# Kernel optimization log

Measured on AMD Instinct MI355X. Metric: run time of the kernel, lower is better.

## Reference

```python
import jax, jax.numpy as jnp
import numpy as np

B, S, D = 1, 2048, 2048
H, KV, HD = 16, 8, 128
GROUP = H // KV
INTER = 6144
L = 2
VOCAB = 32000
EPS = 1e-6
THETA = 10000.0


def _rope_tables(seq_len, head_dim, theta):
    inv_freq = 1.0 / theta ** (np.arange(0, head_dim, 2, dtype=np.float32) / head_dim)
    pos = np.arange(seq_len, dtype=np.float32)
    ang = pos[:, None] * inv_freq[None, :]
    ang = np.concatenate([ang, ang], axis=1)  # [S, HD]
    return jnp.asarray(np.cos(ang)), jnp.asarray(np.sin(ang))


def setup_inputs() -> dict:
    key = jax.random.key(0)
    ks = jax.random.split(key, 16)
    sd = 0.02
    inp = {}
    inp['input_ids'] = jax.random.randint(ks[0], (B, S), 0, VOCAB, dtype=jnp.int32)
    inp['mask'] = jnp.triu(jnp.ones((S, S), dtype=bool), k=1)  # True = masked (future)
    cos, sin = _rope_tables(S, HD, THETA)
    inp['cos'], inp['sin'] = cos, sin
    inp['embed'] = jax.random.normal(ks[1], (VOCAB, D), jnp.float32) * sd
    # torch Linear convention: weight [out, in], y = x @ W.T
    inp['q_w'] = jax.random.normal(ks[2], (L, H * HD, D), jnp.float32) * sd
    inp['k_w'] = jax.random.normal(ks[3], (L, KV * HD, D), jnp.float32) * sd
    inp['v_w'] = jax.random.normal(ks[4], (L, KV * HD, D), jnp.float32) * sd
    inp['o_w'] = jax.random.normal(ks[5], (L, D, H * HD), jnp.float32) * sd
    inp['qn_scale'] = jnp.ones((L, HD), jnp.float32)
    inp['kn_scale'] = jnp.ones((L, HD), jnp.float32)
    inp['ln1_scale'] = jnp.ones((L, D), jnp.float32)
    inp['ln2_scale'] = jnp.ones((L, D), jnp.float32)
    inp['gate_w'] = jax.random.normal(ks[6], (L, INTER, D), jnp.float32) * sd
    inp['up_w'] = jax.random.normal(ks[7], (L, INTER, D), jnp.float32) * sd
    inp['down_w'] = jax.random.normal(ks[8], (L, D, INTER), jnp.float32) * sd
    return inp


def rms_norm(x, scale, eps=EPS):
    xf = x.astype(jnp.float32)
    var = jnp.mean(xf * xf, axis=-1, keepdims=True)
    return (xf * jax.lax.rsqrt(var + eps) * scale).astype(x.dtype)


def apply_rope(x, cos, sin):
    # x: [B, heads, S, HD]
    s = x.shape[2]
    hd = x.shape[-1]
    x1, x2 = x[..., : hd // 2], x[..., hd // 2:]
    rotated = jnp.concatenate([-x2, x1], axis=-1)
    return x * cos[None, None, :s] + rotated * sin[None, None, :s]


def decoder_layer(h, p, mask, cos, sin):
    (q_w, k_w, v_w, o_w, qn, kn, ln1, ln2, gate_w, up_w, down_w) = p
    b, s, _ = h.shape
    x = rms_norm(h, ln1)
    q = (x @ q_w.T).reshape(b, s, H, HD).transpose(0, 2, 1, 3)   # [B,H,S,HD]
    k = (x @ k_w.T).reshape(b, s, KV, HD).transpose(0, 2, 1, 3)  # [B,KV,S,HD]
    v = (x @ v_w.T).reshape(b, s, KV, HD).transpose(0, 2, 1, 3)
    q = rms_norm(q, qn)
    k = rms_norm(k, kn)
    q = apply_rope(q, cos, sin)
    k = apply_rope(k, cos, sin)
    kr = jnp.repeat(k, GROUP, axis=1)  # GQA head expansion
    vr = jnp.repeat(v, GROUP, axis=1)
    scores = jnp.einsum('bhqd,bhkd->bhqk', q, kr) / jnp.sqrt(jnp.float32(HD))
    scores = jnp.where(mask[None, None], -jnp.inf, scores)
    attn = jax.nn.softmax(scores, axis=-1)
    ctx = jnp.einsum('bhqk,bhkd->bhqd', attn, vr)
    ctx = ctx.transpose(0, 2, 1, 3).reshape(b, s, H * HD)
    h = h + ctx @ o_w.T
    x = rms_norm(h, ln2)
    mlp = (jax.nn.silu(x @ gate_w.T) * (x @ up_w.T)) @ down_w.T
    return h + mlp


def reference(input_ids, mask, cos, sin, embed, q_w, k_w, v_w, o_w,
              qn_scale, kn_scale, ln1_scale, ln2_scale, gate_w, up_w, down_w):
    h = embed[input_ids]  # [B, S, D]
    params = (q_w, k_w, v_w, o_w, qn_scale, kn_scale, ln1_scale, ln2_scale,
              gate_w, up_w, down_w)

    def body(carry, p):
        return decoder_layer(carry, p, mask, cos, sin), None

    h, _ = jax.lax.scan(body, h, params)
    return h
```

## Files before the change

### kernel.cpp

```cpp
#include <hip/hip_runtime.h>
#include <hip/hip_bf16.h>

static constexpr int SEQ   = 2048;
static constexpr int DM    = 2048;
static constexpr int NHEAD = 16;
static constexpr int NKVH  = 8;
static constexpr int HDIM  = 128;
static constexpr int FFN   = 6144;
static constexpr int NLAYER = 2;
static constexpr float EPSV = 1e-6f;
static constexpr int QKVN  = NHEAD * HDIM + 2 * NKVH * HDIM;

typedef __attribute__((ext_vector_type(8))) short bf16x8;
typedef __attribute__((ext_vector_type(4))) float f32x4;

__device__ __forceinline__ float wave_sum(float v) {
#pragma unroll
    for (int o = 32; o > 0; o >>= 1) v += __shfl_xor(v, o);
    return v;
}

__device__ __forceinline__ void gload16(const void* g, void* l) {
    __builtin_amdgcn_global_load_lds(
        (const __attribute__((address_space(1))) void*)g,
        (__attribute__((address_space(3))) void*)l,
        16, 0, 0);
}

__global__ void embed_k(const int* __restrict__ ids, const float* __restrict__ emb,
                        float* __restrict__ h) {
    const int s = blockIdx.x;
    const long src = (long)ids[s] * DM;
    for (int t = threadIdx.x; t < DM; t += 256)
        h[(long)s * DM + t] = emb[src + t];
}

__global__ void rmsnorm_k(const float* __restrict__ in, const float* __restrict__ g,
                          __hip_bfloat16* __restrict__ out) {
    const int row = blockIdx.x;
    const float* r = in + (long)row * DM;
    const int tid = threadIdx.x;
    float v[8];
    float ss = 0.f;
#pragma unroll
    for (int t = 0; t < 8; ++t) { v[t] = r[tid + t * 256]; ss += v[t] * v[t]; }
    ss = wave_sum(ss);
    __shared__ float sp[4];
    if ((tid & 63) == 0) sp[tid >> 6] = ss;
    __syncthreads();
    ss = sp[0] + sp[1] + sp[2] + sp[3];
    const float inv = rsqrtf(ss * (1.f / DM) + EPSV);
    __hip_bfloat16* o_ = out + (long)row * DM;
#pragma unroll
    for (int t = 0; t < 8; ++t) {
        const int j = tid + t * 256;
        o_[j] = __float2bfloat16(v[t] * inv * g[j]);
    }
}

__global__ void rmsnorm_res4_k(const __hip_bfloat16* __restrict__ part, long n,
                               float* __restrict__ h, const float* __restrict__ g,
                               __hip_bfloat16* __restrict__ x) {
    const int row = blockIdx.x;
    const int tid = threadIdx.x;
    const long base = (long)row * DM + tid * 8;
    float v[8];
    *(float4*)&v[0] = *(const float4*)(h + base);
    *(float4*)&v[4] = *(const float4*)(h + base + 4);
#pragma unroll
    for (int z = 0; z < 4; ++z) {
        union { bf16x8 vv; __hip_bfloat16 e[8]; } p;
        p.vv = *(const bf16x8*)(part + (long)z * n + base);
#pragma unroll
        for (int j = 0; j < 8; ++j) v[j] += __bfloat162float(p.e[j]);
    }
    *(float4*)(h + base) = *(float4*)&v[0];
    *(float4*)(h + base + 4) = *(float4*)&v[4];
    float ss = 0.f;
#pragma unroll
    for (int j = 0; j < 8; ++j) ss += v[j] * v[j];
    ss = wave_sum(ss);
    __shared__ float sp[4];
    if ((tid & 63) == 0) sp[tid >> 6] = ss;
    __syncthreads();
    ss = sp[0] + sp[1] + sp[2] + sp[3];
    const float inv = rsqrtf(ss * (1.f / DM) + EPSV);
    const float4 g0 = *(const float4*)(g + tid * 8);
    const float4 g1 = *(const float4*)(g + tid * 8 + 4);
    union { bf16x8 vv; __hip_bfloat16 e[8]; } o;
    o.e[0] = __float2bfloat16(v[0] * inv * g0.x); o.e[1] = __float2bfloat16(v[1] * inv * g0.y);
    o.e[2] = __float2bfloat16(v[2] * inv * g0.z); o.e[3] = __float2bfloat16(v[3] * inv * g0.w);
    o.e[4] = __float2bfloat16(v[4] * inv * g1.x); o.e[5] = __float2bfloat16(v[5] * inv * g1.y);
    o.e[6] = __float2bfloat16(v[6] * inv * g1.z); o.e[7] = __float2bfloat16(v[7] * inv * g1.w);
    *(bf16x8*)(x + base) = o.vv;
}

__global__ void red4res_k(const __hip_bfloat16* __restrict__ p, long n, float* __restrict__ h) {
    const long i = ((long)blockIdx.x * 256 + threadIdx.x) * 8;
    float v[8];
    *(float4*)&v[0] = *(const float4*)(h + i);
    *(float4*)&v[4] = *(const float4*)(h + i + 4);
#pragma unroll
    for (int z = 0; z < 4; ++z) {
        union { bf16x8 vv; __hip_bfloat16 e[8]; } b;
        b.vv = *(const bf16x8*)(p + (long)z * n + i);
#pragma unroll
        for (int j = 0; j < 8; ++j) v[j] += __bfloat162float(b.e[j]);
    }
    *(float4*)(h + i) = *(float4*)&v[0];
    *(float4*)(h + i + 4) = *(float4*)&v[4];
}

__global__ void qknorm_rope_k(const __hip_bfloat16* __restrict__ in, long zStride, int inOff,
                              const float* __restrict__ ns,
                              const float* __restrict__ cosT, const float* __restrict__ sinT,
                              __hip_bfloat16* __restrict__ out, int nheads) {
    const int idx = blockIdx.x * 4 + (threadIdx.x >> 6);
    const int lane = threadIdx.x & 63;
    const int s = idx / nheads;
    const int hh = idx - s * nheads;
    const long base = (long)s * QKVN + inOff + hh * HDIM;
    const float x1 = __bfloat162float(in[base + lane]) + __bfloat162float(in[zStride + base + lane]);
    const float x2 = __bfloat162float(in[base + lane + 64]) + __bfloat162float(in[zStride + base + lane + 64]);
    float ss = wave_sum(x1 * x1 + x2 * x2);
    const float inv = rsqrtf(ss * (1.f / HDIM) + EPSV);
    const float n1 = x1 * inv * ns[lane];
    const float n2 = x2 * inv * ns[lane + 64];
    const float c1 = cosT[s * HDIM + lane],      c2 = cosT[s * HDIM + 64 + lane];
    const float s1 = sinT[s * HDIM + lane],      s2 = sinT[s * HDIM + 64 + lane];
    __hip_bfloat16* w = out + ((long)hh * SEQ + s) * HDIM;
    w[lane]      = __float2bfloat16(n1 * c1 - n2 * s1);
    w[lane + 64] = __float2bfloat16(n2 * c2 + n1 * s2);
}

__global__ void vtrans_k(const __hip_bfloat16* __restrict__ vf, long zStride, int colOff,
                         __hip_bfloat16* __restrict__ vt) {
    __shared__ float tile[64][65];
    const int s0 = blockIdx.x * 64, d0 = blockIdx.y * 64, kv = blockIdx.z;
    const int lane = threadIdx.x & 63, part = threadIdx.x >> 6;
    for (int r = part; r < 64; r += 4) {
        const long idx = (long)(s0 + r) * QKVN + colOff + kv * HDIM + d0 + lane;
        tile[r][lane] = __bfloat162float(vf[idx]) + __bfloat162float(vf[zStride + idx]);
    }
    __syncthreads();
    for (int r = part; r < 64; r += 4)
        vt[((long)kv * HDIM + d0 + r) * SEQ + s0 + lane] = __float2bfloat16(tile[lane][r]);
}

__global__ void silu_red2_k(const __hip_bfloat16* __restrict__ p, long n,
                            __hip_bfloat16* __restrict__ out) {
    const long i = ((long)blockIdx.x * 256 + threadIdx.x) * 8;
    union { bf16x8 v; __hip_bfloat16 e[8]; } g0, g1, u0, u1, o;
    g0.v = *(const bf16x8*)(p + i);
    g1.v = *(const bf16x8*)(p + n + i);
    u0.v = *(const bf16x8*)(p + 2 * n + i);
    u1.v = *(const bf16x8*)(p + 3 * n + i);
#pragma unroll
    for (int j = 0; j < 8; ++j) {
        const float g = __bfloat162float(g0.e[j]) + __bfloat162float(g1.e[j]);
        const float u = __bfloat162float(u0.e[j]) + __bfloat162float(u1.e[j]);
        const float sv = g / (1.f + __expf(-g));
        o.e[j] = __float2bfloat16(sv * u);
    }
    *(bf16x8*)(out + i) = o.v;
}

__global__ __launch_bounds__(256)
void flash_k(const __hip_bfloat16* __restrict__ qb, const __hip_bfloat16* __restrict__ kb,
             const __hip_bfloat16* __restrict__ vt, __hip_bfloat16* __restrict__ ctx) {
    __shared__ __align__(16) char ks[2][16384];
    __shared__ __align__(16) char vs[2][16384];
    __shared__ __align__(16) char ps[4][2048];

    const int tid = threadIdx.x;
    const int lane = tid & 63;
    const int wid = tid >> 6;
    const int l15 = lane & 15;
    const int l4 = lane >> 4;

    const int h = blockIdx.y;
    const int kvh = h >> 1;
    const float scale = 0.0883883476483184405f;

    auto stageK = [&](int buf, int kt) {
        const __hip_bfloat16* kg = kb + ((long)kvh * SEQ + kt * 64) * HDIM;
#pragma unroll
        for (int i = 0; i < 4; ++i) {
            const int c = i * 256 + tid;
            const int r = c >> 4, s = c & 15;
            gload16(kg + (long)r * HDIM + ((s ^ (r & 7)) * 8), ks[buf] + c * 16);
        }
    };
    auto stageV = [&](int buf, int kt) {
        const __hip_bfloat16* vg = vt + (long)kvh * HDIM * SEQ + kt * 64;
#pragma unroll
        for (int i = 0; i < 4; ++i) {
            const int c = i * 256 + tid;
            const int r = c >> 3, s = c & 7;
            gload16(vg + (long)r * SEQ + ((s ^ (r & 7)) * 8), vs[buf] + c * 16);
        }
    };

#pragma unroll
    for (int half = 0; half < 2; ++half) {
        const int x = half ? 31 - blockIdx.x : blockIdx.x;
        const int q0 = x * 64;
        const int nkt = x + 1;

        bf16x8 aq[4];
        {
            const __hip_bfloat16* qg = qb + ((long)h * SEQ + q0 + wid * 16 + l15) * HDIM + l4 * 8;
#pragma unroll
            for (int kk = 0; kk < 4; ++kk) aq[kk] = *(const bf16x8*)(qg + kk * 32);
        }

        float mreg[4], lreg[4];
#pragma unroll
        for (int j = 0; j < 4; ++j) { mreg[j] = -3.0e38f; lreg[j] = 0.f; }
        f32x4 oacc[8];
#pragma unroll
        for (int n = 0; n < 8; ++n) oacc[n] = (f32x4){0.f, 0.f, 0.f, 0.f};

        stageK(0, 0); stageV(0, 0);
        asm volatile("s_waitcnt vmcnt(0)" ::: "memory");
        __builtin_amdgcn_s_barrier();

        for (int kt = 0; kt < nkt; ++kt) {
            const int cur = kt & 1;
            if (kt + 1 < nkt) { stageK(cur ^ 1, kt + 1); stageV(cur ^ 1, kt + 1); }

            f32x4 sac[4];
#pragma unroll
            for (int n = 0; n < 4; ++n) sac[n] = (f32x4){0.f, 0.f, 0.f, 0.f};
            __builtin_amdgcn_s_setprio(1);
#pragma unroll
            for (int kk = 0; kk < 4; ++kk) {
#pragma unroll
                for (int n = 0; n < 4; ++n) {
                    const int r = n * 16 + l15;
                    const bf16x8 bk = *(const bf16x8*)(ks[cur] + r * 256 + (((kk * 4 + l4) ^ (r & 7)) << 4));
                    sac[n] = __builtin_amdgcn_mfma_f32_16x16x32_bf16(aq[kk], bk, sac[n], 0, 0, 0);
                }
            }
            __builtin_amdgcn_s_setprio(0);

            const bool diag = (kt + 1 == nkt);
            float mnj[4], alj[4];
#pragma unroll
            for (int j = 0; j < 4; ++j) {
                float mx = -3.0e38f;
#pragma unroll
                for (int n = 0; n < 4; ++n) {
                    float v = sac[n][j] * scale;
                    if (diag && (n * 16 + l15 > wid * 16 + l4 * 4 + j)) v = -3.0e38f;
                    sac[n][j] = v;
                    mx = fmaxf(mx, v);
                }
#pragma unroll
                for (int o = 1; o < 16; o <<= 1) mx = fmaxf(mx, __shfl_xor(mx, o));
                const float mn = fmaxf(mreg[j], mx);
                mnj[j] = mn;
                alj[j] = __expf(mreg[j] - mn);
                mreg[j] = mn;
            }
#pragma unroll
            for (int j = 0; j < 4; ++j) {
                float rs = 0.f;
#pragma unroll
                for (int n = 0; n < 4; ++n) {
                    const float e = __expf(sac[n][j] - mnj[j]);
                    sac[n][j] = e;
                    rs += e;
                }
#pragma unroll
                for (int o = 1; o < 16; o <<= 1) rs += __shfl_xor(rs, o);
                lreg[j] = lreg[j] * alj[j] + rs;
#pragma unroll
                for (int n2 = 0; n2 < 8; ++n2) oacc[n2][j] *= alj[j];
            }

            char* pw = ps[wid];
#pragma unroll
            for (int n = 0; n < 4; ++n)
#pragma unroll
                for (int j = 0; j < 4; ++j) {
                    const int r = l4 * 4 + j;
                    const int col = n * 16 + l15;
                    *(__hip_bfloat16*)(pw + r * 128 + (((col >> 3) ^ (r & 7)) << 4) + (col & 7) * 2) =
                        __float2bfloat16(sac[n][j]);
                }
            asm volatile("s_waitcnt lgkmcnt(0)" ::: "memory");
            __builtin_amdgcn_sched_barrier(0);
            __builtin_amdgcn_s_setprio(1);
#pragma unroll
            for (int kk = 0; kk < 2; ++kk) {
                const bf16x8 ap = *(const bf16x8*)(pw + l15 * 128 + (((kk * 4 + l4) ^ (l15 & 7)) << 4));
#pragma unroll
                for (int n2 = 0; n2 < 8; ++n2) {
                    const int r = n2 * 16 + l15;
                    const bf16x8 bv = *(const bf16x8*)(vs[cur] + r * 128 + (((kk * 4 + l4) ^ (r & 7)) << 4));
                    oacc[n2] = __builtin_amdgcn_mfma_f32_16x16x32_bf16(ap, bv, oacc[n2], 0, 0, 0);
                }
            }
            __builtin_amdgcn_s_setprio(0);

            asm volatile("s_waitcnt vmcnt(0)" ::: "memory");
            __builtin_amdgcn_s_barrier();
        }

#pragma unroll
        for (int j = 0; j < 4; ++j) {
            const float inv = 1.f / lreg[j];
            const long rowb = (long)(q0 + wid * 16 + l4 * 4 + j) * (NHEAD * HDIM) + h * HDIM;
#pragma unroll
            for (int n2 = 0; n2 < 8; ++n2)
                ctx[rowb + n2 * 16 + l15] = __float2bfloat16(oacc[n2][j] * inv);
        }
    }
}

template <int ZSEL>
__global__ __launch_bounds__(512, 2)
void g8p(const __hip_bfloat16* __restrict__ A,
         const float* __restrict__ Ba, const float* __restrict__ Bb, const float* __restrict__ Bc,
         __hip_bfloat16* __restrict__ C, int kLen, int ldA, int ldB, int ldC,
         int seg1, int seg2, long cZStride, int kZStride, int zDiv) {
    __shared__ __align__(16) char sA[2][2][16384];
    __shared__ __align__(16) char sB[2][2][16384];

    const int tid = threadIdx.x;
    const int lane = tid & 63;
    const int wid = tid >> 6;
    const int wr = wid >> 2;
    const int wc = wid & 3;
    const int l15 = lane & 15;
    const int l4 = lane >> 4;

    const int row0 = blockIdx.y * 256;
    const int col0 = blockIdx.x * 256;
    const int z = blockIdx.z;

    const float* B;
    int colB;
    if (ZSEL) {
        B = (z / zDiv) ? Bb : Ba; colB = col0;
    } else {
        if (col0 >= seg2)      { B = Bc; colB = col0 - seg2; }
        else if (col0 >= seg1) { B = Bb; colB = col0 - seg1; }
        else                   { B = Ba; colB = col0; }
    }
    const long cOff = (long)z * cZStride;
    const int k0z = (z % zDiv) * kZStride;
    const int nk = kLen / 64;

    f32x4 acc[8][4];
#pragma unroll
    for (int m = 0; m < 8; ++m)
#pragma unroll
        for (int n = 0; n < 4; ++n)
            acc[m][n] = (f32x4){0.f, 0.f, 0.f, 0.f};

    auto stageA = [&](int half, int kt) {
        const __hip_bfloat16* base = A + (long)(row0 + half * 128) * ldA;
        char* dst = sA[kt & 1][half];
        const int k0 = k0z + kt * 64;
#pragma unroll
        for (int i = 0; i < 2; ++i) {
            const int c = i * 512 + tid;
            const int r = c >> 3, s = c & 7;
            gload16(base + (long)r * ldA + k0 + ((s ^ (r & 7)) * 8), dst + c * 16);
        }
    };
    auto loadB = [&](float4* rb, int half, int kt) {
        const int k0 = k0z + kt * 64;
        const float* base = B + (long)(colB + half * 128) * ldB + k0;
#pragma unroll
        for (int i = 0; i < 2; ++i) {
            const int sidx = i * 512 + tid;
            const int r = sidx >> 3, q = sidx & 7;
            const float* p = base + (long)r * ldB + q * 8;
            rb[i * 2]     = *(const float4*)p;
            rb[i * 2 + 1] = *(const float4*)(p + 4);
        }
    };
    auto writeB = [&](const float4* rb, int half, int kt) {
        char* dst = sB[kt & 1][half];
#pragma unroll
        for (int i = 0; i < 2; ++i) {
            const int sidx = i * 512 + tid;
            const int r = sidx >> 3, q = sidx & 7;
            union { bf16x8 v; __hip_bfloat16 e[8]; } u;
            const float* f = (const float*)&rb[i * 2];
#pragma unroll
            for (int j = 0; j < 8; ++j) u.e[j] = __float2bfloat16(f[j]);
            *(bf16x8*)(dst + (r * 8 + (q ^ (r & 7))) * 16) = u.v;
        }
    };

    auto readA = [&](int buf, int p, int mm, int ks) -> bf16x8 {
        const int r = p * 32 + mm * 16 + l15;
        const int q = ks * 4 + l4;
        return *(const bf16x8*)(sA[buf][wr] + r * 128 + ((q ^ (r & 7)) << 4));
    };
    auto readB = [&](int buf, int nn, int ks) -> bf16x8 {
        const int r = (wc & 1) * 64 + nn * 16 + l15;
        const int q = ks * 4 + l4;
        return *(const bf16x8*)(sB[buf][wc >> 1] + r * 128 + ((q ^ (r & 7)) << 4));
    };

    float4 rb0[4], rb1[4];
    loadB(rb0, 0, 0);
    stageA(0, 0); stageA(1, 0);
    asm volatile("s_waitcnt vmcnt(4)" ::: "memory");
    writeB(rb0, 0, 0);
    loadB(rb1, 1, 0);
    asm volatile("s_waitcnt vmcnt(0)" ::: "memory");
    writeB(rb1, 1, 0);
    if (nk > 1) { loadB(rb0, 0, 1); loadB(rb1, 1, 1); }
    asm volatile("s_waitcnt lgkmcnt(0)" ::: "memory");
    __builtin_amdgcn_sched_barrier(0);
    __builtin_amdgcn_s_barrier();

    bf16x8 bfrag[4][2];
    for (int t = 0; t < nk; ++t) {
        const int cur = t & 1;

        {
            bf16x8 a0[2][2], a1[2][2];
            a0[0][0] = readA(cur, 0, 0, 0); a0[0][1] = readA(cur, 0, 0, 1);
            a0[1][0] = readA(cur, 0, 1, 0); a0[1][1] = readA(cur, 0, 1, 1);
            a1[0][0] = readA(cur, 1, 0, 0); a1[0][1] = readA(cur, 1, 0, 1);
            a1[1][0] = readA(cur, 1, 1, 0); a1[1][1] = readA(cur, 1, 1, 1);
#pragma unroll
            for (int n = 0; n < 4; ++n) {
                bfrag[n][0] = readB(cur, n, 0);
                bfrag[n][1] = readB(cur, n, 1);
            }
            if (t + 1 < nk) {
                writeB(rb0, 0, t + 1);
                writeB(rb1, 1, t + 1);
                stageA(0, t + 1);
                stageA(1, t + 1);
            }
            asm volatile("s_waitcnt lgkmcnt(8)" ::: "memory");
            __builtin_amdgcn_sched_barrier(0);
            __builtin_amdgcn_s_barrier();
            asm volatile("s_waitcnt lgkmcnt(0)" ::: "memory");
            __builtin_amdgcn_sched_barrier(0);

            __builtin_amdgcn_s_setprio(1);
#pragma unroll
            for (int ks = 0; ks < 2; ++ks) {
#pragma unroll
                for (int mm = 0; mm < 2; ++mm)
#pragma unroll
                    for (int n = 0; n < 4; ++n)
                        acc[mm][n] = __builtin_amdgcn_mfma_f32_16x16x32_bf16(
                            a0[mm][ks], bfrag[n][ks], acc[mm][n], 0, 0, 0);
#pragma unroll
                for (int mm = 0; mm < 2; ++mm)
#pragma unroll
                    for (int n = 0; n < 4; ++n)
                        acc[2 + mm][n] = __builtin_amdgcn_mfma_f32_16x16x32_bf16(
                            a1[mm][ks], bfrag[n][ks], acc[2 + mm][n], 0, 0, 0);
            }
            __builtin_amdgcn_s_setprio(0);
            __builtin_amdgcn_sched_barrier(0);
            __builtin_amdgcn_s_barrier();
        }

        {
            bf16x8 a2[2][2], a3[2][2];
            a2[0][0] = readA(cur, 2, 0, 0); a2[0][1] = readA(cur, 2, 0, 1);
            a2[1][0] = readA(cur, 2, 1, 0); a2[1][1] = readA(cur, 2, 1, 1);
            a3[0][0] = readA(cur, 3, 0, 0); a3[0][1] = readA(cur, 3, 0, 1);
            a3[1][0] = readA(cur, 3, 1, 0); a3[1][1] = readA(cur, 3, 1, 1);
            if (t + 2 < nk) {
                loadB(rb0, 0, t + 2);
                loadB(rb1, 1, t + 2);
            }
            __builtin_amdgcn_sched_barrier(0);
            if (t + 2 < nk)      asm volatile("s_waitcnt vmcnt(8)" ::: "memory");
            else if (t + 1 < nk) asm volatile("s_waitcnt vmcnt(0)" ::: "memory");
            __builtin_amdgcn_s_barrier();
            asm volatile("s_waitcnt lgkmcnt(0)" ::: "memory");
            __builtin_amdgcn_sched_barrier(0);

            __builtin_amdgcn_s_setprio(1);
#pragma unroll
            for (int ks = 0; ks < 2; ++ks) {
#pragma unroll
                for (int mm = 0; mm < 2; ++mm)
#pragma unroll
                    for (int n = 0; n < 4; ++n)
                        acc[4 + mm][n] = __builtin_amdgcn_mfma_f32_16x16x32_bf16(
                            a2[mm][ks], bfrag[n][ks], acc[4 + mm][n], 0, 0, 0);
#pragma unroll
                for (int mm = 0; mm < 2; ++mm)
#pragma unroll
                    for (int n = 0; n < 4; ++n)
                        acc[6 + mm][n] = __builtin_amdgcn_mfma_f32_16x16x32_bf16(
                            a3[mm][ks], bfrag[n][ks], acc[6 + mm][n], 0, 0, 0);
            }
            __builtin_amdgcn_s_setprio(0);
            __builtin_amdgcn_sched_barrier(0);
            __builtin_amdgcn_s_barrier();
        }
    }

#pragma unroll
    for (int m = 0; m < 8; ++m) {
#pragma unroll
        for (int n = 0; n < 4; ++n) {
            const int rb = row0 + wr * 128 + m * 16 + l4 * 4;
            const int cc = col0 + wc * 64 + n * 16 + l15;
#pragma unroll
            for (int j = 0; j < 4; ++j)
                C[cOff + (long)(rb + j) * ldC + cc] = __float2bfloat16(acc[m][n][j]);
        }
    }
}

extern "C" void kernel_launch(void* const* d_in, const int* in_sizes, int n_in,
                              void* d_out, int out_size, void* d_ws, size_t ws_size,
                              hipStream_t stream) {
    const int*   ids  = (const int*)d_in[0];
    const float* cosT = (const float*)d_in[2];
    const float* sinT = (const float*)d_in[3];
    const float* emb  = (const float*)d_in[4];
    const float* q_w  = (const float*)d_in[5];
    const float* k_w  = (const float*)d_in[6];
    const float* v_w  = (const float*)d_in[7];
    const float* o_w  = (const float*)d_in[8];
    const float* qn   = (const float*)d_in[9];
    const float* kn   = (const float*)d_in[10];
    const float* ln1  = (const float*)d_in[11];
    const float* ln2  = (const float*)d_in[12];
    const float* gw   = (const float*)d_in[13];
    const float* uw   = (const float*)d_in[14];
    const float* dw   = (const float*)d_in[15];

    char* W = (char*)d_ws;
    size_t off = 0;
    auto take = [&](size_t nb) { char* p = W + off; off += (nb + 255) & ~(size_t)255; return p; };

    float*          h    = (float*)          take((size_t)SEQ * DM * 4);
    __hip_bfloat16* x    = (__hip_bfloat16*) take((size_t)SEQ * DM * 2);
    __hip_bfloat16* part = (__hip_bfloat16*) take((size_t)4 * SEQ * FFN * 2);
    __hip_bfloat16* qb   = (__hip_bfloat16*) take((size_t)NHEAD * SEQ * HDIM * 2);
    __hip_bfloat16* kb   = (__hip_bfloat16*) take((size_t)NKVH * SEQ * HDIM * 2);
    __hip_bfloat16* vt   = (__hip_bfloat16*) take((size_t)NKVH * HDIM * SEQ * 2);
    __hip_bfloat16* ctx  = (__hip_bfloat16*) take((size_t)SEQ * NHEAD * HDIM * 2);
    __hip_bfloat16* go   = (__hip_bfloat16*) take((size_t)SEQ * FFN * 2);
    if (off > ws_size) return;

    embed_k<<<SEQ, 256, 0, stream>>>(ids, emb, h);
    rmsnorm_k<<<SEQ, 256, 0, stream>>>(h, ln1, x);

    const long nQKV = (long)SEQ * QKVN;
    const long nDM  = (long)SEQ * DM;
    const long nFFN = (long)SEQ * FFN;
    const int BIG = 1 << 30;

    for (int l = 0; l < NLAYER; ++l) {
        const float* qwl = q_w + (size_t)l * (NHEAD * HDIM) * DM;
        const float* kwl = k_w + (size_t)l * (NKVH * HDIM) * DM;
        const float* vwl = v_w + (size_t)l * (NKVH * HDIM) * DM;
        const float* owl = o_w + (size_t)l * DM * (NHEAD * HDIM);
        const float* gwl = gw  + (size_t)l * FFN * DM;
        const float* uwl = uw  + (size_t)l * FFN * DM;
        const float* dwl = dw  + (size_t)l * DM * FFN;

        g8p<0><<<dim3(QKVN / 256, SEQ / 256, 2), 512, 0, stream>>>(
            x, qwl, kwl, vwl, part, DM / 2, DM, DM, QKVN,
            NHEAD * HDIM, NHEAD * HDIM + NKVH * HDIM, nQKV, DM / 2, 2);

        qknorm_rope_k<<<SEQ * NHEAD / 4, 256, 0, stream>>>(
            part, nQKV, 0, qn + l * HDIM, cosT, sinT, qb, NHEAD);
        qknorm_rope_k<<<SEQ * NKVH / 4, 256, 0, stream>>>(
            part, nQKV, NHEAD * HDIM, kn + l * HDIM, cosT, sinT, kb, NKVH);
        vtrans_k<<<dim3(SEQ / 64, HDIM / 64, NKVH), 256, 0, stream>>>(
            part, nQKV, NHEAD * HDIM + NKVH * HDIM, vt);

        flash_k<<<dim3(16, NHEAD), 256, 0, stream>>>(qb, kb, vt, ctx);

        g8p<0><<<dim3(DM / 256, SEQ / 256, 4), 512, 0, stream>>>(
            ctx, owl, owl, owl, part, (NHEAD * HDIM) / 4, NHEAD * HDIM, NHEAD * HDIM, DM,
            BIG, BIG, nDM, (NHEAD * HDIM) / 4, 4);
        rmsnorm_res4_k<<<SEQ, 256, 0, stream>>>(part, nDM, h, ln2 + l * DM, x);

        g8p<1><<<dim3(FFN / 256, SEQ / 256, 4), 512, 0, stream>>>(
            x, gwl, uwl, uwl, part, DM / 2, DM, DM, FFN,
            BIG, BIG, nFFN, DM / 2, 2);
        silu_red2_k<<<(int)(nFFN / 2048), 256, 0, stream>>>(part, nFFN, go);

        g8p<0><<<dim3(DM / 256, SEQ / 256, 4), 512, 0, stream>>>(
            go, dwl, dwl, dwl, part, FFN / 4, FFN, FFN, DM,
            BIG, BIG, nDM, FFN / 4, 4);
        if (l + 1 < NLAYER)
            rmsnorm_res4_k<<<SEQ, 256, 0, stream>>>(part, nDM, h, ln1 + (l + 1) * DM, x);
        else
            red4res_k<<<(int)(nDM / 2048), 256, 0, stream>>>(part, nDM, h);
    }

    hipMemcpyAsync(d_out, h, (size_t)out_size * sizeof(float), hipMemcpyDeviceToDevice, stream);
}
```

Baseline: 842.7 us.

## Fuse small kernels and skip flash rescale when row max unchanged

Merges the embedding gather with the first RMSNorm, fuses the Q/K norm-rope and V transpose into one launch, and writes the final residual sum directly to the output buffer instead of copying it. Together these remove several launches and the final device copy. In the flash attention loop, the exp-rescale of the accumulator is skipped when no row maximum grew anywhere in the wave. That branch adds divergence checks in exchange for fewer multiplies and exps.

```diff
diff --git a/kernel.cpp b/kernel.cpp
--- a/kernel.cpp
+++ b/kernel.cpp
@@ -27,30 +27,28 @@
         16, 0, 0);
 }
 
-__global__ void embed_k(const int* __restrict__ ids, const float* __restrict__ emb,
-                        float* __restrict__ h) {
-    const int s = blockIdx.x;
-    const long src = (long)ids[s] * DM;
-    for (int t = threadIdx.x; t < DM; t += 256)
-        h[(long)s * DM + t] = emb[src + t];
-}
-
-__global__ void rmsnorm_k(const float* __restrict__ in, const float* __restrict__ g,
-                          __hip_bfloat16* __restrict__ out) {
+__global__ void embed_rms_k(const int* __restrict__ ids, const float* __restrict__ emb,
+                            const float* __restrict__ g, float* __restrict__ h,
+                            __hip_bfloat16* __restrict__ x) {
     const int row = blockIdx.x;
-    const float* r = in + (long)row * DM;
+    const long src = (long)ids[row] * DM;
     const int tid = threadIdx.x;
     float v[8];
     float ss = 0.f;
 #pragma unroll
-    for (int t = 0; t < 8; ++t) { v[t] = r[tid + t * 256]; ss += v[t] * v[t]; }
+    for (int t = 0; t < 8; ++t) {
+        const int j = tid + t * 256;
+        v[t] = emb[src + j];
+        h[(long)row * DM + j] = v[t];
+        ss += v[t] * v[t];
+    }
     ss = wave_sum(ss);
     __shared__ float sp[4];
     if ((tid & 63) == 0) sp[tid >> 6] = ss;
     __syncthreads();
     ss = sp[0] + sp[1] + sp[2] + sp[3];
     const float inv = rsqrtf(ss * (1.f / DM) + EPSV);
-    __hip_bfloat16* o_ = out + (long)row * DM;
+    __hip_bfloat16* o_ = x + (long)row * DM;
 #pragma unroll
     for (int t = 0; t < 8; ++t) {
         const int j = tid + t * 256;
@@ -95,7 +93,8 @@
     *(bf16x8*)(x + base) = o.vv;
 }
 
-__global__ void red4res_k(const __hip_bfloat16* __restrict__ p, long n, float* __restrict__ h) {
+__global__ void red4out_k(const __hip_bfloat16* __restrict__ p, long n,
+                          const float* __restrict__ h, float* __restrict__ out) {
     const long i = ((long)blockIdx.x * 256 + threadIdx.x) * 8;
     float v[8];
     *(float4*)&v[0] = *(const float4*)(h + i);
@@ -107,44 +106,57 @@
 #pragma unroll
         for (int j = 0; j < 8; ++j) v[j] += __bfloat162float(b.e[j]);
     }
-    *(float4*)(h + i) = *(float4*)&v[0];
-    *(float4*)(h + i + 4) = *(float4*)&v[4];
-}
-
-__global__ void qknorm_rope_k(const __hip_bfloat16* __restrict__ in, long zStride, int inOff,
-                              const float* __restrict__ ns,
-                              const float* __restrict__ cosT, const float* __restrict__ sinT,
-                              __hip_bfloat16* __restrict__ out, int nheads) {
-    const int idx = blockIdx.x * 4 + (threadIdx.x >> 6);
-    const int lane = threadIdx.x & 63;
-    const int s = idx / nheads;
-    const int hh = idx - s * nheads;
-    const long base = (long)s * QKVN + inOff + hh * HDIM;
-    const float x1 = __bfloat162float(in[base + lane]) + __bfloat162float(in[zStride + base + lane]);
-    const float x2 = __bfloat162float(in[base + lane + 64]) + __bfloat162float(in[zStride + base + lane + 64]);
-    float ss = wave_sum(x1 * x1 + x2 * x2);
-    const float inv = rsqrtf(ss * (1.f / HDIM) + EPSV);
-    const float n1 = x1 * inv * ns[lane];
-    const float n2 = x2 * inv * ns[lane + 64];
-    const float c1 = cosT[s * HDIM + lane],      c2 = cosT[s * HDIM + 64 + lane];
-    const float s1 = sinT[s * HDIM + lane],      s2 = sinT[s * HDIM + 64 + lane];
-    __hip_bfloat16* w = out + ((long)hh * SEQ + s) * HDIM;
-    w[lane]      = __float2bfloat16(n1 * c1 - n2 * s1);
-    w[lane + 64] = __float2bfloat16(n2 * c2 + n1 * s2);
-}
-
-__global__ void vtrans_k(const __hip_bfloat16* __restrict__ vf, long zStride, int colOff,
-                         __hip_bfloat16* __restrict__ vt) {
+    *(float4*)(out + i) = *(float4*)&v[0];
+    *(float4*)(out + i + 4) = *(float4*)&v[4];
+}
+
+__global__ void qkv_post_k(const __hip_bfloat16* __restrict__ in, long zStride,
+                           const float* __restrict__ qns, const float* __restrict__ kns,
+                           const float* __restrict__ cosT, const float* __restrict__ sinT,
+                           __hip_bfloat16* __restrict__ qb, __hip_bfloat16* __restrict__ kb,
+                           __hip_bfloat16* __restrict__ vt) {
     __shared__ float tile[64][65];
-    const int s0 = blockIdx.x * 64, d0 = blockIdx.y * 64, kv = blockIdx.z;
-    const int lane = threadIdx.x & 63, part = threadIdx.x >> 6;
-    for (int r = part; r < 64; r += 4) {
-        const long idx = (long)(s0 + r) * QKVN + colOff + kv * HDIM + d0 + lane;
-        tile[r][lane] = __bfloat162float(vf[idx]) + __bfloat162float(vf[zStride + idx]);
-    }
-    __syncthreads();
-    for (int r = part; r < 64; r += 4)
-        vt[((long)kv * HDIM + d0 + r) * SEQ + s0 + lane] = __float2bfloat16(tile[lane][r]);
+    const int bid = blockIdx.x;
+    constexpr int QB = SEQ * NHEAD / 4;
+    constexpr int KB = QB + SEQ * NKVH / 4;
+
+    if (bid < KB) {
+        const bool isQ = bid < QB;
+        const int nheads = isQ ? NHEAD : NKVH;
+        const int inOff = isQ ? 0 : NHEAD * HDIM;
+        const float* ns = isQ ? qns : kns;
+        __hip_bfloat16* out = isQ ? qb : kb;
+        const int idx = (isQ ? bid : bid - QB) * 4 + (threadIdx.x >> 6);
+        const int lane = threadIdx.x & 63;
+        const int s = idx / nheads;
+        const int hh = idx - s * nheads;
+        const long base = (long)s * QKVN + inOff + hh * HDIM;
+        const float x1 = __bfloat162float(in[base + lane]) + __bfloat162float(in[zStride + base + lane]);
+        const float x2 = __bfloat162float(in[base + lane + 64]) + __bfloat162float(in[zStride + base + lane + 64]);
+        float ss = wave_sum(x1 * x1 + x2 * x2);
+        const float inv = rsqrtf(ss * (1.f / HDIM) + EPSV);
+        const float n1 = x1 * inv * ns[lane];
+        const float n2 = x2 * inv * ns[lane + 64];
+        const float c1 = cosT[s * HDIM + lane],      c2 = cosT[s * HDIM + 64 + lane];
+        const float s1 = sinT[s * HDIM + lane],      s2 = sinT[s * HDIM + 64 + lane];
+        __hip_bfloat16* w = out + ((long)hh * SEQ + s) * HDIM;
+        w[lane]      = __float2bfloat16(n1 * c1 - n2 * s1);
+        w[lane + 64] = __float2bfloat16(n2 * c2 + n1 * s2);
+    } else {
+        const int lin = bid - KB;
+        const int s0 = (lin & 31) * 64;
+        const int d0 = ((lin >> 5) & 1) * 64;
+        const int kv = lin >> 6;
+        const int colOff = NHEAD * HDIM + NKVH * HDIM;
+        const int lane = threadIdx.x & 63, part = threadIdx.x >> 6;
+        for (int r = part; r < 64; r += 4) {
+            const long idx = (long)(s0 + r) * QKVN + colOff + kv * HDIM + d0 + lane;
+            tile[r][lane] = __bfloat162float(in[idx]) + __bfloat162float(in[zStride + idx]);
+        }
+        __syncthreads();
+        for (int r = part; r < 64; r += 4)
+            vt[((long)kv * HDIM + d0 + r) * SEQ + s0 + lane] = __float2bfloat16(tile[lane][r]);
+    }
 }
 
 __global__ void silu_red2_k(const __hip_bfloat16* __restrict__ p, long n,
@@ -245,38 +257,56 @@
             __builtin_amdgcn_s_setprio(0);
 
             const bool diag = (kt + 1 == nkt);
-            float mnj[4], alj[4];
+            float mx[4];
+            bool grew = false;
 #pragma unroll
             for (int j = 0; j < 4; ++j) {
-                float mx = -3.0e38f;
+                float m_ = -3.0e38f;
 #pragma unroll
                 for (int n = 0; n < 4; ++n) {
                     float v = sac[n][j] * scale;
                     if (diag && (n * 16 + l15 > wid * 16 + l4 * 4 + j)) v = -3.0e38f;
                     sac[n][j] = v;
-                    mx = fmaxf(mx, v);
+                    m_ = fmaxf(m_, v);
                 }
 #pragma unroll
-                for (int o = 1; o < 16; o <<= 1) mx = fmaxf(mx, __shfl_xor(mx, o));
-                const float mn = fmaxf(mreg[j], mx);
-                mnj[j] = mn;
-                alj[j] = __expf(mreg[j] - mn);
-                mreg[j] = mn;
-            }
-#pragma unroll
-            for (int j = 0; j < 4; ++j) {
-                float rs = 0.f;
-#pragma unroll
-                for (int n = 0; n < 4; ++n) {
-                    const float e = __expf(sac[n][j] - mnj[j]);
-                    sac[n][j] = e;
-                    rs += e;
+                for (int o = 1; o < 16; o <<= 1) m_ = fmaxf(m_, __shfl_xor(m_, o));
+                mx[j] = m_;
+                grew = grew || (m_ > mreg[j]);
+            }
+            if (__any(grew)) {
+#pragma unroll
+                for (int j = 0; j < 4; ++j) {
+                    const float mn = fmaxf(mreg[j], mx[j]);
+                    const float al = __expf(mreg[j] - mn);
+                    mreg[j] = mn;
+                    float rs = 0.f;
+#pragma unroll
+                    for (int n = 0; n < 4; ++n) {
+                        const float e = __expf(sac[n][j] - mn);
+                        sac[n][j] = e;
+                        rs += e;
+                    }
+#pragma unroll
+                    for (int o = 1; o < 16; o <<= 1) rs += __shfl_xor(rs, o);
+                    lreg[j] = lreg[j] * al + rs;
+#pragma unroll
+                    for (int n2 = 0; n2 < 8; ++n2) oacc[n2][j] *= al;
                 }
-#pragma unroll
-                for (int o = 1; o < 16; o <<= 1) rs += __shfl_xor(rs, o);
-                lreg[j] = lreg[j] * alj[j] + rs;
-#pragma unroll
-                for (int n2 = 0; n2 < 8; ++n2) oacc[n2][j] *= alj[j];
+            } else {
+#pragma unroll
+                for (int j = 0; j < 4; ++j) {
+                    float rs = 0.f;
+#pragma unroll
+                    for (int n = 0; n < 4; ++n) {
+                        const float e = __expf(sac[n][j] - mreg[j]);
+                        sac[n][j] = e;
+                        rs += e;
+                    }
+#pragma unroll
+                    for (int o = 1; o < 16; o <<= 1) rs += __shfl_xor(rs, o);
+                    lreg[j] += rs;
+                }
             }
 
             char* pw = ps[wid];
@@ -554,13 +584,13 @@
     __hip_bfloat16* go   = (__hip_bfloat16*) take((size_t)SEQ * FFN * 2);
     if (off > ws_size) return;
 
-    embed_k<<<SEQ, 256, 0, stream>>>(ids, emb, h);
-    rmsnorm_k<<<SEQ, 256, 0, stream>>>(h, ln1, x);
+    embed_rms_k<<<SEQ, 256, 0, stream>>>(ids, emb, ln1, h, x);
 
     const long nQKV = (long)SEQ * QKVN;
     const long nDM  = (long)SEQ * DM;
     const long nFFN = (long)SEQ * FFN;
     const int BIG = 1 << 30;
+    const int POST_BLOCKS = SEQ * NHEAD / 4 + SEQ * NKVH / 4 + (SEQ / 64) * (HDIM / 64) * NKVH;
 
     for (int l = 0; l < NLAYER; ++l) {
         const float* qwl = q_w + (size_t)l * (NHEAD * HDIM) * DM;
@@ -575,12 +605,8 @@
             x, qwl, kwl, vwl, part, DM / 2, DM, DM, QKVN,
             NHEAD * HDIM, NHEAD * HDIM + NKVH * HDIM, nQKV, DM / 2, 2);
 
-        qknorm_rope_k<<<SEQ * NHEAD / 4, 256, 0, stream>>>(
-            part, nQKV, 0, qn + l * HDIM, cosT, sinT, qb, NHEAD);
-        qknorm_rope_k<<<SEQ * NKVH / 4, 256, 0, stream>>>(
-            part, nQKV, NHEAD * HDIM, kn + l * HDIM, cosT, sinT, kb, NKVH);
-        vtrans_k<<<dim3(SEQ / 64, HDIM / 64, NKVH), 256, 0, stream>>>(
-            part, nQKV, NHEAD * HDIM + NKVH * HDIM, vt);
+        qkv_post_k<<<POST_BLOCKS, 256, 0, stream>>>(
+            part, nQKV, qn + l * HDIM, kn + l * HDIM, cosT, sinT, qb, kb, vt);
 
         flash_k<<<dim3(16, NHEAD), 256, 0, stream>>>(qb, kb, vt, ctx);
 
@@ -600,8 +626,6 @@
         if (l + 1 < NLAYER)
             rmsnorm_res4_k<<<SEQ, 256, 0, stream>>>(part, nDM, h, ln1 + (l + 1) * DM, x);
         else
-            red4res_k<<<(int)(nDM / 2048), 256, 0, stream>>>(part, nDM, h);
-    }
-
-    hipMemcpyAsync(d_out, h, (size_t)out_size * sizeof(float), hipMemcpyDeviceToDevice, stream);
-}
+            red4out_k<<<(int)(nDM / 2048), 256, 0, stream>>>(part, nDM, h, (float*)d_out);
+    }
+}
```

Result: no change. 831.4 us (-1.3%).
